# Performance work log

Measured on AMD Instinct MI355X. Metric: run time of the kernel, lower is better.

The kernel has to match this reference:

```python
import jax, jax.numpy as jnp
import numpy as np

N, E, DIN, DOUT = 40000, 640000, 128, 256
BN_EPS = 1e-5  # torch BatchNorm1d default eps


def setup_inputs() -> dict:
    key = jax.random.key(0)
    ks = jax.random.split(key, 16)
    x = jax.random.normal(ks[0], (N, DIN), jnp.float32)
    edge_index = jax.random.randint(ks[1], (2, E), 0, N, dtype=jnp.int32)
    s1 = 1.0 / np.sqrt(DIN)
    s2 = 1.0 / np.sqrt(DOUT)
    return {
        "x": x,
        "edge_index": edge_index,
        "eps": jnp.zeros((), jnp.float32),  # GINConv train_eps init = 0
        "W1": jax.random.normal(ks[2], (DIN, DOUT), jnp.float32) * s1,
        "b1": jnp.zeros((DOUT,), jnp.float32),
        "g1": jnp.ones((DOUT,), jnp.float32),
        "bt1": jnp.zeros((DOUT,), jnp.float32),
        "m1": jax.random.normal(ks[3], (DOUT,), jnp.float32) * 0.1,
        "v1": jax.random.uniform(ks[4], (DOUT,), jnp.float32, 0.5, 1.5),
        "W2": jax.random.normal(ks[5], (DOUT, DOUT), jnp.float32) * s2,
        "b2": jnp.zeros((DOUT,), jnp.float32),
        "g2": jnp.ones((DOUT,), jnp.float32),
        "bt2": jnp.zeros((DOUT,), jnp.float32),
        "m2": jax.random.normal(ks[6], (DOUT,), jnp.float32) * 0.1,
        "v2": jax.random.uniform(ks[7], (DOUT,), jnp.float32, 0.5, 1.5),
        "Wres": jax.random.normal(ks[8], (DIN, DOUT), jnp.float32) * s1,
    }


def _bn(h, g, b, m, v):
    # inference-mode BatchNorm1d with running stats
    return (h - m) * jax.lax.rsqrt(v + BN_EPS) * g + b


def reference(x, edge_index, eps, W1, b1, g1, bt1, m1, v1,
              W2, b2, g2, bt2, m2, v2, Wres):
    src, dst = edge_index[0], edge_index[1]
    # GIN sum aggregation: messages x[src] scatter-added at dst
    agg = jax.ops.segment_sum(x[src], dst, num_segments=N)  # [N, DIN]
    h = (1.0 + eps) * x + agg
    h = jax.nn.relu(_bn(h @ W1 + b1, g1, bt1, m1, v1))       # [N, DOUT]
    h = jax.nn.relu(_bn(h @ W2 + b2, g2, bt2, m2, v2))       # [N, DOUT]
    # dropout is identity in eval mode; residual projection since DIN != DOUT
    return jax.nn.relu(h + x @ Wres)
```

## Files before the change

kernel.cpp:

```cpp
#include <hip/hip_runtime.h>

#define NN 40000
#define NPAD 40064
#define EE 640000
#define KDIN 128
#define KDOUT 256

#define NB 157
#define CAP 6144

typedef __attribute__((ext_vector_type(8))) short bf16x8;
typedef __attribute__((ext_vector_type(4))) float f32x4;

static __device__ __forceinline__ unsigned short f2bf(float f) {
    union { float f; unsigned int u; } v; v.f = f;
    unsigned int r = (v.u + 0x7FFFu + ((v.u >> 16) & 1u)) >> 16;
    return (unsigned short)r;
}
static __device__ __forceinline__ float bf2f(unsigned short h) {
    union { unsigned int u; float f; } v; v.u = ((unsigned int)h) << 16;
    return v.f;
}

#define PREP_GRID 3021
__global__ __launch_bounds__(256) void k_prep(
    const float* __restrict__ x,
    const float* __restrict__ W1, const float* __restrict__ W2,
    const float* __restrict__ Wres,
    ushort* __restrict__ xb, ushort* __restrict__ wt_all,
    int* __restrict__ cur, ushort* __restrict__ hb) {
    int b = blockIdx.x, tid = threadIdx.x;
    if (b < 2504) {
        int i = b * 256 + tid;
        int row = i >> 4;
        uint4 o = {0, 0, 0, 0};
        if (row < NN) {
            const float4* xp = (const float4*)x + (size_t)i * 2;
            float4 a = xp[0], c = xp[1];
            o.x = (unsigned)f2bf(a.x) | ((unsigned)f2bf(a.y) << 16);
            o.y = (unsigned)f2bf(a.z) | ((unsigned)f2bf(a.w) << 16);
            o.z = (unsigned)f2bf(c.x) | ((unsigned)f2bf(c.y) << 16);
            o.w = (unsigned)f2bf(c.z) | ((unsigned)f2bf(c.w) << 16);
        }
        if (row < NPAD) *(uint4*)(xb + (size_t)i * 8) = o;
    } else if (b < 3016) {
        int j = (b - 2504) * 256 + tid;
        if (j < 32768) {
            int c = j >> 7, r = j & 127;
            wt_all[j] = f2bf(W1[r * KDOUT + c]);
        } else if (j < 98304) {
            int j2 = j - 32768;
            int c = j2 >> 8, r = j2 & 255;
            wt_all[j] = f2bf(W2[r * KDOUT + c]);
        } else {
            int j3 = j - 98304;
            int c = j3 >> 7, r = j3 & 127;
            wt_all[j] = f2bf(Wres[r * KDOUT + c]);
        }
    } else if (b < 3020) {
        int idx = (b - 3016) * 256 + tid;
        ((uint4*)(hb + (size_t)NN * KDIN))[idx] = (uint4){0, 0, 0, 0};
    } else {
        if (tid < NB) cur[tid] = 0;
    }
}

__global__ __launch_bounds__(256) void k_binA(const int* __restrict__ ei,
                                              int* __restrict__ cur,
                                              unsigned int* __restrict__ recs) {
    __shared__ int cnt[160], lstart[160], lcur[160], gbase[160];
    __shared__ int sw[256];
    __shared__ unsigned int lrec[4096];
    __shared__ int laddr[4096];
    int tid = threadIdx.x;
    int e0 = blockIdx.x * 4096;
    int e1 = min(e0 + 4096, EE);
    int ns = e1 - e0;

    if (tid < NB) cnt[tid] = 0;
    __syncthreads();
    for (int s = tid; s < ns; s += 256)
        atomicAdd(&cnt[ei[EE + e0 + s] >> 8], 1);
    __syncthreads();
    sw[tid] = (tid < NB) ? cnt[tid] : 0;
    __syncthreads();
    for (int off = 1; off < 256; off <<= 1) {
        int add = (tid >= off) ? sw[tid - off] : 0;
        __syncthreads();
        sw[tid] += add;
        __syncthreads();
    }
    if (tid < NB) {
        int st = sw[tid] - cnt[tid];
        lstart[tid] = st;
        lcur[tid] = st;
        gbase[tid] = atomicAdd(&cur[tid], cnt[tid]);
    }
    __syncthreads();
    for (int s = tid; s < ns; s += 256) {
        int e = e0 + s;
        int src = ei[e];
        int dst = ei[EE + e];
        int b = dst >> 8;
        int p = atomicAdd(&lcur[b], 1);
        lrec[p] = ((unsigned int)(dst & 255) << 16) | (unsigned int)src;
        laddr[p] = b * CAP + gbase[b] + (p - lstart[b]);
    }
    __syncthreads();
    for (int s = tid; s < ns; s += 256)
        recs[laddr[s]] = lrec[s];
}

__global__ __launch_bounds__(256) void k_aggB(const unsigned int* __restrict__ recs,
                                              const int* __restrict__ cur,
                                              const ushort* __restrict__ xb,
                                              const float* __restrict__ eps,
                                              ushort* __restrict__ hb) {
    __shared__ ushort lsrc[CAP];
    __shared__ int lcnt[256], lst[256], lcur[256];
    __shared__ int sw[256];
    int tid = threadIdx.x;
    int b = blockIdx.x >> 1, half = blockIdx.x & 1;
    int cnt = cur[b];
    const unsigned int* rb = recs + (size_t)b * CAP;

    lcnt[tid] = 0;
    __syncthreads();
    for (int s = tid; s < cnt; s += 256)
        atomicAdd(&lcnt[rb[s] >> 16], 1);
    __syncthreads();
    sw[tid] = lcnt[tid];
    __syncthreads();
    for (int off = 1; off < 256; off <<= 1) {
        int add = (tid >= off) ? sw[tid - off] : 0;
        __syncthreads();
        sw[tid] += add;
        __syncthreads();
    }
    int excl = sw[tid] - lcnt[tid];
    lst[tid] = excl;
    lcur[tid] = excl;
    __syncthreads();
    for (int s = tid; s < cnt; s += 256) {
        unsigned int r = rb[s];
        int p = atomicAdd(&lcur[r >> 16], 1);
        lsrc[p] = (ushort)(r & 0xffff);
    }
    __syncthreads();

    int g = tid >> 3, lane = tid & 7;
    float s1 = 1.0f + eps[0];
    for (int d = g; d < 256; d += 32) {
        int node = b * 256 + d;
        if (node >= NN) continue;
        int st = lst[d], en = st + lcnt[d];
        const uint4* xrow = (const uint4*)(xb + (size_t)node * KDIN) + half * 8;
        uint4 me = xrow[lane];
        float a[8], a2[8];
        a[0] = bf2f((ushort)(me.x & 0xffff)) * s1; a[1] = bf2f((ushort)(me.x >> 16)) * s1;
        a[2] = bf2f((ushort)(me.y & 0xffff)) * s1; a[3] = bf2f((ushort)(me.y >> 16)) * s1;
        a[4] = bf2f((ushort)(me.z & 0xffff)) * s1; a[5] = bf2f((ushort)(me.z >> 16)) * s1;
        a[6] = bf2f((ushort)(me.w & 0xffff)) * s1; a[7] = bf2f((ushort)(me.w >> 16)) * s1;
#pragma unroll
        for (int i = 0; i < 8; ++i) a2[i] = 0.f;
        int e = st;
        for (; e + 1 < en; e += 2) {
            int s0 = lsrc[e], sB = lsrc[e + 1];
            uint4 v0 = *((const uint4*)(xb + (size_t)s0 * KDIN) + half * 8 + lane);
            uint4 v1 = *((const uint4*)(xb + (size_t)sB * KDIN) + half * 8 + lane);
            a[0] += bf2f((ushort)(v0.x & 0xffff)); a[1] += bf2f((ushort)(v0.x >> 16));
            a[2] += bf2f((ushort)(v0.y & 0xffff)); a[3] += bf2f((ushort)(v0.y >> 16));
            a[4] += bf2f((ushort)(v0.z & 0xffff)); a[5] += bf2f((ushort)(v0.z >> 16));
            a[6] += bf2f((ushort)(v0.w & 0xffff)); a[7] += bf2f((ushort)(v0.w >> 16));
            a2[0] += bf2f((ushort)(v1.x & 0xffff)); a2[1] += bf2f((ushort)(v1.x >> 16));
            a2[2] += bf2f((ushort)(v1.y & 0xffff)); a2[3] += bf2f((ushort)(v1.y >> 16));
            a2[4] += bf2f((ushort)(v1.z & 0xffff)); a2[5] += bf2f((ushort)(v1.z >> 16));
            a2[6] += bf2f((ushort)(v1.w & 0xffff)); a2[7] += bf2f((ushort)(v1.w >> 16));
        }
        if (e < en) {
            int s0 = lsrc[e];
            uint4 v0 = *((const uint4*)(xb + (size_t)s0 * KDIN) + half * 8 + lane);
            a[0] += bf2f((ushort)(v0.x & 0xffff)); a[1] += bf2f((ushort)(v0.x >> 16));
            a[2] += bf2f((ushort)(v0.y & 0xffff)); a[3] += bf2f((ushort)(v0.y >> 16));
            a[4] += bf2f((ushort)(v0.z & 0xffff)); a[5] += bf2f((ushort)(v0.z >> 16));
            a[6] += bf2f((ushort)(v0.w & 0xffff)); a[7] += bf2f((ushort)(v0.w >> 16));
        }
#pragma unroll
        for (int i = 0; i < 8; ++i) a[i] += a2[i];
        uint4 o;
        o.x = (unsigned)f2bf(a[0]) | ((unsigned)f2bf(a[1]) << 16);
        o.y = (unsigned)f2bf(a[2]) | ((unsigned)f2bf(a[3]) << 16);
        o.z = (unsigned)f2bf(a[4]) | ((unsigned)f2bf(a[5]) << 16);
        o.w = (unsigned)f2bf(a[6]) | ((unsigned)f2bf(a[7]) << 16);
        *((uint4*)(hb + (size_t)node * KDIN) + half * 8 + lane) = o;
    }
}


#define STAGE_WT(Wt_, Kc_, K2_)                                                 \
    for (int id = tid; id < BNT * (K2_) / 16; id += 256) {                      \
        int c = id / ((K2_) / 16);                                              \
        int koff = (id % ((K2_) / 16)) * 16;                                    \
        uint4 v = *(const uint4*)((const char*)((Wt_) + (size_t)(ncol0 + c) * (Kc_)) + koff); \
        *(uint4*)((char*)s + c * (K2_) + (koff ^ ((c & 7) << 4))) = v;          \
    }

#define MM_LOOP(A_, Kc_, K2_, acc0_, acc1_)                                     \
    {                                                                           \
        const char* a0p = (const char*)((A_) + (size_t)r0 * (Kc_)) + lq * 16;   \
        const char* a1p = a0p + 16 * (Kc_) * 2;                                 \
        for (int k0 = 0; k0 < (Kc_); k0 += 32) {                                \
            bf16x8 a0 = *(const bf16x8*)(a0p + k0 * 2);                         \
            bf16x8 a1 = *(const bf16x8*)(a1p + k0 * 2);                         \
            int kb = (k0 + lq * 8) * 2;                                         \
            _Pragma("unroll")                                                   \
            for (int nt = 0; nt < 8; ++nt) {                                    \
                int c = nt * 16 + l15;                                          \
                bf16x8 b = *(const bf16x8*)((const char*)s + c * (K2_) + (kb ^ ((c & 7) << 4))); \
                acc0_[nt] = __builtin_amdgcn_mfma_f32_16x16x32_bf16(a0, b, acc0_[nt], 0, 0, 0); \
                acc1_[nt] = __builtin_amdgcn_mfma_f32_16x16x32_bf16(a1, b, acc1_[nt], 0, 0, 0); \
            }                                                                   \
        }                                                                       \
    }

#define BNT 128

__global__ __launch_bounds__(256) void k_mm1(
    const ushort* __restrict__ A, const ushort* __restrict__ Wt,
    const float* __restrict__ bb, const float* __restrict__ g,
    const float* __restrict__ bt, const float* __restrict__ m,
    const float* __restrict__ vv, ushort* __restrict__ C) {
    __shared__ ushort s[BNT * 128];
    int tid = threadIdx.x;
    int bm = blockIdx.x >> 1, bn = blockIdx.x & 1;
    int ncol0 = bn * BNT;
    STAGE_WT(Wt, 128, 256);
    __syncthreads();
    int wid = tid >> 6, lane = tid & 63;
    int l15 = lane & 15, lq = lane >> 4;
    int r0 = bm * 128 + wid * 32 + l15;
    f32x4 acc0[8] = {}, acc1[8] = {};
    MM_LOOP(A, 128, 256, acc0, acc1);
#pragma unroll
    for (int nt = 0; nt < 8; ++nt) {
        int col = ncol0 + nt * 16 + l15;
        float sc = g[col] * rsqrtf(vv[col] + 1e-5f);
        float bo = (bb[col] - m[col]) * sc + bt[col];
        int rb = bm * 128 + wid * 32 + lq * 4;
#pragma unroll
        for (int r = 0; r < 4; ++r) {
            C[(size_t)(rb + r) * KDOUT + col] = f2bf(fmaxf(acc0[nt][r] * sc + bo, 0.f));
            C[(size_t)(rb + 16 + r) * KDOUT + col] = f2bf(fmaxf(acc1[nt][r] * sc + bo, 0.f));
        }
    }
}

__global__ __launch_bounds__(256) void k_mm2(
    const ushort* __restrict__ H1, const ushort* __restrict__ W2t,
    const ushort* __restrict__ X, const ushort* __restrict__ Wrt,
    const float* __restrict__ bb, const float* __restrict__ g,
    const float* __restrict__ bt, const float* __restrict__ m,
    const float* __restrict__ vv, float* __restrict__ OUT) {
    __shared__ ushort s[BNT * 256];
    int tid = threadIdx.x;
    int bm = blockIdx.x >> 1, bn = blockIdx.x & 1;
    int ncol0 = bn * BNT;
    int wid = tid >> 6, lane = tid & 63;
    int l15 = lane & 15, lq = lane >> 4;
    int r0 = bm * 128 + wid * 32 + l15;

    STAGE_WT(W2t, 256, 512);
    __syncthreads();
    f32x4 acc0[8] = {}, acc1[8] = {};
    MM_LOOP(H1, 256, 512, acc0, acc1);

    __syncthreads();
    STAGE_WT(Wrt, 128, 256);
    __syncthreads();
    f32x4 acd0[8] = {}, acd1[8] = {};
    MM_LOOP(X, 128, 256, acd0, acd1);

#pragma unroll
    for (int nt = 0; nt < 8; ++nt) {
        int col = ncol0 + nt * 16 + l15;
        float sc = g[col] * rsqrtf(vv[col] + 1e-5f);
        float bo = (bb[col] - m[col]) * sc + bt[col];
        int rb = bm * 128 + wid * 32 + lq * 4;
#pragma unroll
        for (int r = 0; r < 4; ++r) {
            int row0 = rb + r, row1 = rb + 16 + r;
            float t0 = fmaxf(acc0[nt][r] * sc + bo, 0.f);
            float t1 = fmaxf(acc1[nt][r] * sc + bo, 0.f);
            if (row0 < NN) OUT[(size_t)row0 * KDOUT + col] = fmaxf(t0 + acd0[nt][r], 0.f);
            if (row1 < NN) OUT[(size_t)row1 * KDOUT + col] = fmaxf(t1 + acd1[nt][r], 0.f);
        }
    }
}

extern "C" void kernel_launch(void* const* d_in, const int* in_sizes, int n_in,
                              void* d_out, int out_size, void* d_ws, size_t ws_size,
                              hipStream_t stream) {
    const float* x    = (const float*)d_in[0];
    const int*   ei   = (const int*)d_in[1];
    const float* eps  = (const float*)d_in[2];
    const float* W1   = (const float*)d_in[3];
    const float* b1   = (const float*)d_in[4];
    const float* g1   = (const float*)d_in[5];
    const float* bt1  = (const float*)d_in[6];
    const float* m1   = (const float*)d_in[7];
    const float* v1   = (const float*)d_in[8];
    const float* W2   = (const float*)d_in[9];
    const float* b2   = (const float*)d_in[10];
    const float* g2   = (const float*)d_in[11];
    const float* bt2  = (const float*)d_in[12];
    const float* m2   = (const float*)d_in[13];
    const float* v2   = (const float*)d_in[14];
    const float* Wres = (const float*)d_in[15];
    float* out = (float*)d_out;

    char* w = (char*)d_ws;
    ushort* xb  = (ushort*)w;                 w += (size_t)NPAD * KDIN * 2;
    ushort* hb  = (ushort*)w;                 w += (size_t)NPAD * KDIN * 2;
    ushort* h1b = (ushort*)w;                 w += (size_t)NPAD * KDOUT * 2;
    ushort* w1t = (ushort*)w;                 w += 256 * 128 * 2;
    ushort* w2t = (ushort*)w;                 w += 256 * 256 * 2;
    ushort* wrt = (ushort*)w;                 w += 256 * 128 * 2;
    int* cur    = (int*)w;                    w += 256 * 4;
    unsigned int* recs = (unsigned int*)w;    w += (size_t)NB * CAP * 4;

    k_prep<<<PREP_GRID, 256, 0, stream>>>(x, W1, W2, Wres, xb, w1t, cur, hb);
    k_binA<<<NB, 256, 0, stream>>>(ei, cur, recs);
    k_aggB<<<NB * 2, 256, 0, stream>>>(recs, cur, xb, eps, hb);

    const int grid = (NPAD / 128) * 2;
    k_mm1<<<grid, 256, 0, stream>>>(hb, w1t, b1, g1, bt1, m1, v1, h1b);
    k_mm2<<<grid, 256, 0, stream>>>(h1b, w2t, xb, wrt, b2, g2, bt2, m2, v2, out);
}
```

Baseline: 124.4 us.

## Split aggregation blocks into node halves and feature quarters for more parallelism

The gather-sum aggregation kernel now launches 8 blocks per destination bin instead of 2. Each block handles half the bin's nodes and one quarter of the feature columns, with 4 lanes per node instead of 8. This raises occupancy and the number of loads in flight on a latency-bound gather over only 314 blocks. In exchange, every block rescans the whole bin record list to build its local CSR, so that counting work is repeated more often, and each gathered row segment is narrower (64 bytes per block).

```diff
diff --git a/kernel.cpp b/kernel.cpp
--- a/kernel.cpp
+++ b/kernel.cpp
@@ -8,6 +8,7 @@
 
 #define NB 157
 #define CAP 6144
+#define CAPH 4096
 
 typedef __attribute__((ext_vector_type(8))) short bf16x8;
 typedef __attribute__((ext_vector_type(4))) float f32x4;
@@ -116,46 +117,53 @@
                                               const ushort* __restrict__ xb,
                                               const float* __restrict__ eps,
                                               ushort* __restrict__ hb) {
-    __shared__ ushort lsrc[CAP];
-    __shared__ int lcnt[256], lst[256], lcur[256];
+    __shared__ ushort lsrc[CAPH];
+    __shared__ int lcnt[128], lst[128], lcur[128];
     __shared__ int sw[256];
     int tid = threadIdx.x;
-    int b = blockIdx.x >> 1, half = blockIdx.x & 1;
+    int bi = blockIdx.x;
+    int b = bi >> 3, nh = (bi >> 2) & 1, q = bi & 3;
     int cnt = cur[b];
     const unsigned int* rb = recs + (size_t)b * CAP;
 
-    lcnt[tid] = 0;
-    __syncthreads();
-    for (int s = tid; s < cnt; s += 256)
-        atomicAdd(&lcnt[rb[s] >> 16], 1);
-    __syncthreads();
-    sw[tid] = lcnt[tid];
-    __syncthreads();
-    for (int off = 1; off < 256; off <<= 1) {
+    if (tid < 128) lcnt[tid] = 0;
+    __syncthreads();
+    for (int s = tid; s < cnt; s += 256) {
+        int d = rb[s] >> 16;
+        if ((d >> 7) == nh) atomicAdd(&lcnt[d & 127], 1);
+    }
+    __syncthreads();
+    sw[tid] = (tid < 128) ? lcnt[tid] : 0;
+    __syncthreads();
+    for (int off = 1; off < 128; off <<= 1) {
         int add = (tid >= off) ? sw[tid - off] : 0;
         __syncthreads();
         sw[tid] += add;
         __syncthreads();
     }
-    int excl = sw[tid] - lcnt[tid];
-    lst[tid] = excl;
-    lcur[tid] = excl;
+    if (tid < 128) {
+        int e = sw[tid] - lcnt[tid];
+        lst[tid] = e;
+        lcur[tid] = e;
+    }
     __syncthreads();
     for (int s = tid; s < cnt; s += 256) {
         unsigned int r = rb[s];
-        int p = atomicAdd(&lcur[r >> 16], 1);
-        lsrc[p] = (ushort)(r & 0xffff);
-    }
-    __syncthreads();
-
-    int g = tid >> 3, lane = tid & 7;
+        int d = r >> 16;
+        if ((d >> 7) == nh) {
+            int p = atomicAdd(&lcur[d & 127], 1);
+            lsrc[p] = (ushort)(r & 0xffff);
+        }
+    }
+    __syncthreads();
+
+    int g = tid >> 2, lane = tid & 3;
     float s1 = 1.0f + eps[0];
-    for (int d = g; d < 256; d += 32) {
-        int node = b * 256 + d;
+    for (int d = g; d < 128; d += 64) {
+        int node = b * 256 + nh * 128 + d;
         if (node >= NN) continue;
         int st = lst[d], en = st + lcnt[d];
-        const uint4* xrow = (const uint4*)(xb + (size_t)node * KDIN) + half * 8;
-        uint4 me = xrow[lane];
+        uint4 me = *((const uint4*)(xb + (size_t)node * KDIN) + q * 4 + lane);
         float a[8], a2[8];
         a[0] = bf2f((ushort)(me.x & 0xffff)) * s1; a[1] = bf2f((ushort)(me.x >> 16)) * s1;
         a[2] = bf2f((ushort)(me.y & 0xffff)) * s1; a[3] = bf2f((ushort)(me.y >> 16)) * s1;
@@ -166,8 +174,8 @@
         int e = st;
         for (; e + 1 < en; e += 2) {
             int s0 = lsrc[e], sB = lsrc[e + 1];
-            uint4 v0 = *((const uint4*)(xb + (size_t)s0 * KDIN) + half * 8 + lane);
-            uint4 v1 = *((const uint4*)(xb + (size_t)sB * KDIN) + half * 8 + lane);
+            uint4 v0 = *((const uint4*)(xb + (size_t)s0 * KDIN) + q * 4 + lane);
+            uint4 v1 = *((const uint4*)(xb + (size_t)sB * KDIN) + q * 4 + lane);
             a[0] += bf2f((ushort)(v0.x & 0xffff)); a[1] += bf2f((ushort)(v0.x >> 16));
             a[2] += bf2f((ushort)(v0.y & 0xffff)); a[3] += bf2f((ushort)(v0.y >> 16));
             a[4] += bf2f((ushort)(v0.z & 0xffff)); a[5] += bf2f((ushort)(v0.z >> 16));
@@ -179,7 +187,7 @@
         }
         if (e < en) {
             int s0 = lsrc[e];
-            uint4 v0 = *((const uint4*)(xb + (size_t)s0 * KDIN) + half * 8 + lane);
+            uint4 v0 = *((const uint4*)(xb + (size_t)s0 * KDIN) + q * 4 + lane);
             a[0] += bf2f((ushort)(v0.x & 0xffff)); a[1] += bf2f((ushort)(v0.x >> 16));
             a[2] += bf2f((ushort)(v0.y & 0xffff)); a[3] += bf2f((ushort)(v0.y >> 16));
             a[4] += bf2f((ushort)(v0.z & 0xffff)); a[5] += bf2f((ushort)(v0.z >> 16));
@@ -192,7 +200,7 @@
         o.y = (unsigned)f2bf(a[2]) | ((unsigned)f2bf(a[3]) << 16);
         o.z = (unsigned)f2bf(a[4]) | ((unsigned)f2bf(a[5]) << 16);
         o.w = (unsigned)f2bf(a[6]) | ((unsigned)f2bf(a[7]) << 16);
-        *((uint4*)(hb + (size_t)node * KDIN) + half * 8 + lane) = o;
+        *((uint4*)(hb + (size_t)node * KDIN) + q * 4 + lane) = o;
     }
 }
 
@@ -330,7 +338,7 @@
 
     k_prep<<<PREP_GRID, 256, 0, stream>>>(x, W1, W2, Wres, xb, w1t, cur, hb);
     k_binA<<<NB, 256, 0, stream>>>(ei, cur, recs);
-    k_aggB<<<NB * 2, 256, 0, stream>>>(recs, cur, xb, eps, hb);
+    k_aggB<<<NB * 8, 256, 0, stream>>>(recs, cur, xb, eps, hb);
 
     const int grid = (NPAD / 128) * 2;
     k_mm1<<<grid, 256, 0, stream>>>(hb, w1t, b1, g1, bt1, m1, v1, h1b);
```

New measurement: 104.6 us. 15.9% less time.
